# Performance work log

Measured on AMD Instinct MI355X. Metric: run time of the kernel, lower is better.

## Reference

```python
import jax, jax.numpy as jnp
import numpy as np

N = 50000        # nodes
E = 800000       # edges (avg degree 16)
C = 64           # node_dim = mid_planes = out_planes
EDGE_DIM = 16    # edge feature dim
S = 8            # share_planes


def setup_inputs() -> dict:
    key = jax.random.key(0)
    ks = jax.random.split(key, 20)

    def lin_w(k, fin, fout):
        return (jax.random.normal(k, (fin, fout), jnp.float32) / np.sqrt(fin)).astype(jnp.float32)

    return {
        "q": jax.random.normal(ks[0], (N, C), jnp.float32),
        "k": jax.random.normal(ks[1], (N, C), jnp.float32),
        "v": jax.random.normal(ks[2], (N, C), jnp.float32),
        "edges": jax.random.normal(ks[3], (E, EDGE_DIM), jnp.float32),
        "edge_index": jax.random.randint(ks[4], (E, 2), 0, N, jnp.int32),
        # linear_q / linear_k / linear_v : C -> C
        "Wq": lin_w(ks[5], C, C), "bq": jnp.zeros((C,), jnp.float32),
        "Wk": lin_w(ks[6], C, C), "bk": jnp.zeros((C,), jnp.float32),
        "Wv": lin_w(ks[7], C, C), "bv": jnp.zeros((C,), jnp.float32),
        # linear_p : EDGE_DIM -> 1
        "Wp": lin_w(ks[8], EDGE_DIM, 1), "bp": jnp.zeros((1,), jnp.float32),
        # linear_w : ReLU -> Linear(C, C//S) -> ReLU -> Linear(C//S, C//S)
        "W1": lin_w(ks[9], C, C // S), "b1": jnp.zeros((C // S,), jnp.float32),
        "W2": lin_w(ks[10], C // S, C // S), "b2": jnp.zeros((C // S,), jnp.float32),
    }


def reference(q, k, v, edges, edge_index,
              Wq, bq, Wk, bk, Wv, bv, Wp, bp, W1, b1, W2, b2):
    src = edge_index[:, 0]  # destination node of aggregation (query side)
    dst = edge_index[:, 1]  # neighbor node (key/value side)

    # node-level projections, then gather per edge
    x_q = (q @ Wq + bq)[src]            # [E, C]
    x_k = (k @ Wk + bk)[dst]            # [E, C]
    x_v = (v @ Wv + bv)[dst]            # [E, C]

    p_r = edges @ Wp + bp               # [E, 1] positional bias

    # vector attention weights (per-edge MLP)
    w = x_k - x_q + p_r                 # [E, C]
    w = jax.nn.relu(w) @ W1 + b1        # [E, C//S]
    w = jax.nn.relu(w) @ W2 + b2        # [E, C//S]
    w = jax.nn.softmax(w, axis=1)       # softmax over shared channel groups

    # weighted values, grouped by share_planes, scatter-sum back to nodes
    msg = ((x_v + p_r).reshape(E, S, C // S) * w[:, None, :]).reshape(E, C)
    return jax.ops.segment_sum(msg, src, num_segments=N)  # [N, C]
```

## Files before the change

kernel.cpp:

```cpp
#include <hip/hip_runtime.h>
#include <hip/hip_fp16.h>

#define N_NODES 50000
#define E_EDGES 800000
#define SCAN_TILE 1024
#define SCAN_NBLK ((N_NODES + SCAN_TILE - 1) / SCAN_TILE)
#define EW_EPT 8

__device__ __forceinline__ float sgpr_f(float x) {
    return __uint_as_float(__builtin_amdgcn_readfirstlane(__float_as_uint(x)));
}

#if defined(__has_builtin)
#if __has_builtin(__builtin_amdgcn_fdot2)
#define HAS_FDOT2 1
#endif
#endif

typedef _Float16 v2h_t __attribute__((ext_vector_type(2)));

__device__ __forceinline__ float fdot2f(__half2 a, __half2 b, float c) {
#ifdef HAS_FDOT2
    return __builtin_amdgcn_fdot2(*reinterpret_cast<v2h_t*>(&a),
                                  *reinterpret_cast<v2h_t*>(&b), c, false);
#else
    const float2 fa = __half22float2(a);
    const float2 fb = __half22float2(b);
    return fmaf(fa.x, fb.x, fmaf(fa.y, fb.y, c));
#endif
}

__device__ __forceinline__ __half2 relu_h2(__half2 x) {
    union { __half2 h; unsigned u; } a, r;
    a.h = x;
    asm("v_pk_max_f16 %0, %1, 0" : "=v"(r.u) : "v"(a.u));
    return r.h;
}

template <int CTRL>
__device__ __forceinline__ float dpp_mov_f32(float x) {
    return __int_as_float(__builtin_amdgcn_update_dpp(
        0, __float_as_int(x), CTRL, 0xF, 0xF, true));
}
template <int CTRL>
__device__ __forceinline__ int dpp_mov_i32(int x) {
    return __builtin_amdgcn_update_dpp(0, x, CTRL, 0xF, 0xF, true);
}
__device__ __forceinline__ float oct_sum(float x) {
    x += dpp_mov_f32<0xB1>(x);
    x += dpp_mov_f32<0x4E>(x);
    x += dpp_mov_f32<0x141>(x);
    return x;
}

__global__ __launch_bounds__(256) void proj_kernel(
    const float* __restrict__ qin, const float* __restrict__ kin, const float* __restrict__ vin,
    const float* __restrict__ Wq, const float* __restrict__ bq,
    const float* __restrict__ Wk, const float* __restrict__ bk,
    const float* __restrict__ Wv, const float* __restrict__ bv,
    __half* __restrict__ xq, __half* __restrict__ xk, __half* __restrict__ xv)
{
    __shared__ float Ws[3 * 4096];
    const int tid = threadIdx.x;
    #pragma unroll
    for (int it = 0; it < 16; ++it) {
        const int idx = it * 256 + tid;
        Ws[idx]        = Wq[idx];
        Ws[4096 + idx] = Wk[idx];
        Ws[8192 + idx] = Wv[idx];
    }
    __syncthreads();

    const int cg = tid & 15;
    const int rg = tid >> 4;
    const int c0 = cg * 4;
    const int base = blockIdx.x * 64 + rg * 4;

    const float* ins[3]  = {qin, kin, vin};
    const float* bs[3]   = {bq, bk, bv};
    __half*      outs[3] = {xq, xk, xv};

    int rowi[4];
    #pragma unroll
    for (int rr = 0; rr < 4; ++rr)
        rowi[rr] = (base + rr < N_NODES) ? (base + rr) : (N_NODES - 1);

    #pragma unroll
    for (int m = 0; m < 3; ++m) {
        const float* in = ins[m];
        const float* Wm = &Ws[m * 4096];
        float4 acc[4];
        const float4 b4 = *reinterpret_cast<const float4*>(&bs[m][c0]);
        #pragma unroll
        for (int rr = 0; rr < 4; ++rr) acc[rr] = b4;

        for (int kk = 0; kk < 64; kk += 4) {
            float4 rv[4];
            #pragma unroll
            for (int rr = 0; rr < 4; ++rr)
                rv[rr] = *reinterpret_cast<const float4*>(&in[rowi[rr] * 64 + kk]);
            #pragma unroll
            for (int dk = 0; dk < 4; ++dk) {
                const float4 w4 = *reinterpret_cast<const float4*>(&Ws[m * 4096 + (kk + dk) * 64 + c0]);
                #pragma unroll
                for (int rr = 0; rr < 4; ++rr) {
                    const float xs = reinterpret_cast<const float*>(&rv[rr])[dk];
                    acc[rr].x = fmaf(xs, w4.x, acc[rr].x);
                    acc[rr].y = fmaf(xs, w4.y, acc[rr].y);
                    acc[rr].z = fmaf(xs, w4.z, acc[rr].z);
                    acc[rr].w = fmaf(xs, w4.w, acc[rr].w);
                }
            }
        }
        #pragma unroll
        for (int rr = 0; rr < 4; ++rr) {
            if (base + rr < N_NODES) {
                union { __half2 h[2]; uint2 u; } pk;
                pk.h[0] = __floats2half2_rn(acc[rr].x, acc[rr].y);
                pk.h[1] = __floats2half2_rn(acc[rr].z, acc[rr].w);
                *reinterpret_cast<uint2*>(&outs[m][(size_t)(base + rr) * 64 + c0]) = pk.u;
            }
        }
    }
}

__global__ __launch_bounds__(256) void scan_sums(
    const int* __restrict__ cnt, int* __restrict__ bsum)
{
    const int tid  = threadIdx.x;
    const int base = blockIdx.x * SCAN_TILE + tid * 4;
    int s = 0;
    if (base + 3 < N_NODES) {
        const int4 t = *reinterpret_cast<const int4*>(&cnt[base]);
        s = t.x + t.y + t.z + t.w;
    } else {
        #pragma unroll
        for (int i = 0; i < 4; ++i)
            if (base + i < N_NODES) s += cnt[base + i];
    }
    #pragma unroll
    for (int d = 1; d < 64; d <<= 1) s += __shfl_xor(s, d);
    __shared__ int ws[4];
    if ((tid & 63) == 0) ws[tid >> 6] = s;
    __syncthreads();
    if (tid == 0) bsum[blockIdx.x] = ws[0] + ws[1] + ws[2] + ws[3];
}

__global__ __launch_bounds__(64) void scan_bsum(int* __restrict__ bsum)
{
    const int lane = threadIdx.x;
    const int v = (lane < SCAN_NBLK) ? bsum[lane] : 0;
    int incl = v;
    #pragma unroll
    for (int d = 1; d < 64; d <<= 1) {
        const int t = __shfl_up(incl, d);
        if (lane >= d) incl += t;
    }
    if (lane < SCAN_NBLK) bsum[lane] = incl - v;
}

__global__ __launch_bounds__(256) void scan_final(
    int* __restrict__ cnt, const int* __restrict__ bsum, int* __restrict__ off)
{
    const int tid  = threadIdx.x;
    const int base = blockIdx.x * SCAN_TILE + tid * 4;

    int v0 = 0, v1 = 0, v2 = 0, v3 = 0;
    if (base + 3 < N_NODES) {
        const int4 t = *reinterpret_cast<const int4*>(&cnt[base]);
        v0 = t.x; v1 = t.y; v2 = t.z; v3 = t.w;
    } else {
        if (base + 0 < N_NODES) v0 = cnt[base + 0];
        if (base + 1 < N_NODES) v1 = cnt[base + 1];
        if (base + 2 < N_NODES) v2 = cnt[base + 2];
        if (base + 3 < N_NODES) v3 = cnt[base + 3];
    }
    const int s = v0 + v1 + v2 + v3;

    int incl = s;
    #pragma unroll
    for (int d = 1; d < 64; d <<= 1) {
        const int t = __shfl_up(incl, d);
        if ((tid & 63) >= d) incl += t;
    }
    __shared__ int wsum[4];
    const int wave = tid >> 6;
    if ((tid & 63) == 63) wsum[wave] = incl;
    __syncthreads();
    int woff = 0;
    #pragma unroll
    for (int w = 0; w < 3; ++w)
        if (w < wave) woff += wsum[w];

    int run = bsum[blockIdx.x] + woff + (incl - s);
    if (base + 0 < N_NODES) { off[base + 0] = run; cnt[base + 0] = run; run += v0; }
    if (base + 1 < N_NODES) { off[base + 1] = run; cnt[base + 1] = run; run += v1; }
    if (base + 2 < N_NODES) { off[base + 2] = run; cnt[base + 2] = run; run += v2; }
    if (base + 3 < N_NODES) { off[base + 3] = run; cnt[base + 3] = run; run += v3; }

    if (blockIdx.x == 0 && tid == 0) off[N_NODES] = E_EDGES;
}

__global__ __launch_bounds__(256) void edge_weights(
    const int* __restrict__ eidx, const float* __restrict__ edges,
    const float* __restrict__ Wp, const float* __restrict__ bp,
    const float* __restrict__ W1, const float* __restrict__ b1,
    const float* __restrict__ W2, const float* __restrict__ b2,
    const __half* __restrict__ xq, const __half* __restrict__ xk,
    int* __restrict__ cnt, uint4* __restrict__ rece)
{
    const int tid  = threadIdx.x;
    const int lane = tid & 63;
    const int o    = lane >> 3;
    const int r    = lane & 7;
    const int wave = tid >> 6;

    __half2 W1h[4][8];
    #pragma unroll
    for (int i = 0; i < 4; ++i) {
        const float4 a0 = *reinterpret_cast<const float4*>(&W1[(8 * r + 2 * i) * 8]);
        const float4 a1 = *reinterpret_cast<const float4*>(&W1[(8 * r + 2 * i) * 8 + 4]);
        const float4 c0 = *reinterpret_cast<const float4*>(&W1[(8 * r + 2 * i + 1) * 8]);
        const float4 c1 = *reinterpret_cast<const float4*>(&W1[(8 * r + 2 * i + 1) * 8 + 4]);
        W1h[i][0] = __floats2half2_rn(a0.x, c0.x);
        W1h[i][1] = __floats2half2_rn(a0.y, c0.y);
        W1h[i][2] = __floats2half2_rn(a0.z, c0.z);
        W1h[i][3] = __floats2half2_rn(a0.w, c0.w);
        W1h[i][4] = __floats2half2_rn(a1.x, c1.x);
        W1h[i][5] = __floats2half2_rn(a1.y, c1.y);
        W1h[i][6] = __floats2half2_rn(a1.z, c1.z);
        W1h[i][7] = __floats2half2_rn(a1.w, c1.w);
    }
    float W2col[8];
    #pragma unroll
    for (int jj = 0; jj < 8; ++jj) W2col[jj] = W2[jj * 8 + r];
    float b1u[8];
    #pragma unroll
    for (int j = 0; j < 8; ++j) b1u[j] = sgpr_f(b1[j]);
    const float b2r = b2[r];
    const float wpA = Wp[2 * r], wpB = Wp[2 * r + 1];
    const float bp0 = sgpr_f(bp[0]);

    const int wb = (blockIdx.x * 4 + wave) * (8 * EW_EPT);

    #pragma unroll
    for (int t = 0; t < EW_EPT; ++t) {
        const int e = wb + t * 8 + o;

        const int2 sd = *reinterpret_cast<const int2*>(&eidx[2 * e]);
        const float2 e2 = *reinterpret_cast<const float2*>(&edges[(size_t)e * 16 + 2 * r]);

        uint4 q4u = *reinterpret_cast<const uint4*>(&xq[(size_t)sd.x * 64 + 8 * r]);
        uint4 k4u = *reinterpret_cast<const uint4*>(&xk[(size_t)sd.y * 64 + 8 * r]);

        float p = fmaf(e2.x, wpA, e2.y * wpB);
        p = oct_sum(p) + bp0;

        const __half2 p2 = __float2half2_rn(p);
        const __half2* qh = reinterpret_cast<const __half2*>(&q4u);
        const __half2* kh = reinterpret_cast<const __half2*>(&k4u);

        float part[8];
        #pragma unroll
        for (int jj = 0; jj < 8; ++jj) part[jj] = 0.f;
        #pragma unroll
        for (int i = 0; i < 4; ++i) {
            const __half2 d = relu_h2(__hadd2(__hsub2(kh[i], qh[i]), p2));
            #pragma unroll
            for (int jj = 0; jj < 8; ++jj)
                part[jj] = fdot2f(d, W1h[i][jj], part[jj]);
        }
        #pragma unroll
        for (int jj = 0; jj < 8; ++jj) part[jj] = oct_sum(part[jj]);

        float h2 = b2r;
        #pragma unroll
        for (int jj = 0; jj < 8; ++jj) {
            const float h1 = fmaxf(part[jj] + b1u[jj], 0.f);
            h2 = fmaf(h1, W2col[jj], h2);
        }

        const float ex = __expf(h2);
        const float sm = oct_sum(ex);
        const float w  = ex / sm;

        const unsigned wu = (unsigned)__float2uint_rn(w * 255.f);
        unsigned word = wu << (8 * (r & 3));
        word |= (unsigned)dpp_mov_i32<0xB1>((int)word);
        word |= (unsigned)dpp_mov_i32<0x4E>((int)word);
        const unsigned other = (unsigned)dpp_mov_i32<0x141>((int)word);

        if (r == 0) {
            uint4 rec;
            rec.x = (unsigned)sd.x | ((unsigned)sd.y << 16);
            rec.y = word;
            rec.z = other;
            rec.w = __float_as_uint(p);
            rece[e] = rec;
        }
        if (r == 1) atomicAdd(&cnt[sd.x], 1);
    }
}

__global__ __launch_bounds__(256) void scatter_kernel(
    const uint4* __restrict__ rece, int* __restrict__ cursor,
    uint4* __restrict__ reccsr)
{
    const int e = blockIdx.x * 256 + threadIdx.x;
    const uint4 rec = rece[e];
    const int src = (int)(rec.x & 0xFFFFu);
    const int pos = atomicAdd(&cursor[src], 1);
    reccsr[pos] = rec;
}

__global__ __launch_bounds__(256) void node_accum(
    const int* __restrict__ off, const uint4* __restrict__ reccsr,
    const __half* __restrict__ xv, float* __restrict__ out)
{
    const int tid  = threadIdx.x;
    const int lane = tid & 63;
    const int grp  = lane >> 4;
    const int sub  = (lane >> 3) & 1;
    const int r    = lane & 7;
    const int wave = tid >> 6;

    const int node = blockIdx.x * 16 + wave * 4 + grp;

    const int beg = off[node];
    const int end = off[node + 1];

    float acc[8];
    #pragma unroll
    for (int i = 0; i < 8; ++i) acc[i] = 0.f;

    int j = beg + sub;
    uint4 rec;
    if (j < end) rec = reccsr[j];

    for (; j < end; j += 2) {
        const uint4 cur = rec;
        const int   dst = (int)(cur.x >> 16);
        const float p   = __uint_as_float(cur.w);

        union { uint4 u; __half2 h[4]; } v4;
        v4.u = *reinterpret_cast<const uint4*>(&xv[(size_t)dst * 64 + 8 * r]);

        if (j + 2 < end) rec = reccsr[j + 2];

        float wf[8];
        #pragma unroll
        for (int i = 0; i < 4; ++i) {
            wf[i]     = (float)((cur.y >> (8 * i)) & 255u);
            wf[4 + i] = (float)((cur.z >> (8 * i)) & 255u);
        }

        #pragma unroll
        for (int i = 0; i < 4; ++i) {
            const float2 fv = __half22float2(v4.h[i]);
            acc[2 * i]     = fmaf(fv.x + p, wf[2 * i],     acc[2 * i]);
            acc[2 * i + 1] = fmaf(fv.y + p, wf[2 * i + 1], acc[2 * i + 1]);
        }
    }

    #pragma unroll
    for (int i = 0; i < 8; ++i)
        acc[i] += __shfl_xor(acc[i], 8);

    if (sub == 0) {
        const float c = 1.f / 255.f;
        float* orow = &out[(size_t)node * 64 + 8 * r];
        *reinterpret_cast<float4*>(orow) =
            make_float4(acc[0] * c, acc[1] * c, acc[2] * c, acc[3] * c);
        *reinterpret_cast<float4*>(orow + 4) =
            make_float4(acc[4] * c, acc[5] * c, acc[6] * c, acc[7] * c);
    }
}

extern "C" void kernel_launch(void* const* d_in, const int* in_sizes, int n_in,
                              void* d_out, int out_size, void* d_ws, size_t ws_size,
                              hipStream_t stream) {
    const float* q     = (const float*)d_in[0];
    const float* k     = (const float*)d_in[1];
    const float* v     = (const float*)d_in[2];
    const float* edges = (const float*)d_in[3];
    const int*   eidx  = (const int*)d_in[4];
    const float* Wq    = (const float*)d_in[5];
    const float* bq    = (const float*)d_in[6];
    const float* Wk    = (const float*)d_in[7];
    const float* bk    = (const float*)d_in[8];
    const float* Wv    = (const float*)d_in[9];
    const float* bv    = (const float*)d_in[10];
    const float* Wp    = (const float*)d_in[11];
    const float* bp    = (const float*)d_in[12];
    const float* W1    = (const float*)d_in[13];
    const float* b1    = (const float*)d_in[14];
    const float* W2    = (const float*)d_in[15];
    const float* b2    = (const float*)d_in[16];
    float* out = (float*)d_out;

    char* ws = (char*)d_ws;
    __half* xq = (__half*)ws;          ws += (size_t)N_NODES * 64 * sizeof(__half);
    __half* xk = (__half*)ws;          ws += (size_t)N_NODES * 64 * sizeof(__half);
    __half* xv = (__half*)ws;          ws += (size_t)N_NODES * 64 * sizeof(__half);
    int* cnt  = (int*)ws;              ws += (size_t)(N_NODES + 64) * sizeof(int);
    int* off  = (int*)ws;              ws += (size_t)(N_NODES + 64) * sizeof(int);
    int* bsum = (int*)ws;              ws += (size_t)64 * sizeof(int);
    uint4* rece   = (uint4*)ws;        ws += (size_t)E_EDGES * sizeof(uint4);
    uint4* reccsr = (uint4*)ws;        ws += (size_t)E_EDGES * sizeof(uint4);

    hipMemsetAsync(cnt, 0, (size_t)N_NODES * sizeof(int), stream);

    proj_kernel<<<dim3((N_NODES + 63) / 64), dim3(256), 0, stream>>>(
        q, k, v, Wq, bq, Wk, bk, Wv, bv, xq, xk, xv);

    edge_weights<<<dim3(E_EDGES / (32 * EW_EPT)), dim3(256), 0, stream>>>(
        eidx, edges, Wp, bp, W1, b1, W2, b2, xq, xk, cnt, rece);

    scan_sums<<<dim3(SCAN_NBLK), dim3(256), 0, stream>>>(cnt, bsum);
    scan_bsum<<<dim3(1), dim3(64), 0, stream>>>(bsum);
    scan_final<<<dim3(SCAN_NBLK), dim3(256), 0, stream>>>(cnt, bsum, off);

    scatter_kernel<<<dim3(E_EDGES / 256), dim3(256), 0, stream>>>(
        rece, cnt, reccsr);

    node_accum<<<dim3(N_NODES / 16), dim3(256), 0, stream>>>(
        off, reccsr, xv, out);
}
```

Before: 172.9 us.

## Build CSR offsets first and scatter edge records directly from edge_weights

Adds a lightweight histogram kernel over edge_index so the scan runs before edge weights are computed, letting edge_weights write each record straight to its CSR slot via the cursor atomic. This removes the intermediate per-edge record buffer and the separate scatter kernel, saving one write and one read of the record array plus a launch. Separately, the projection kernel now stores weights in LDS as packed halves and uses fdot2 on half-converted inputs, halving LDS traffic and FMA count at the cost of fp16 input rounding in the projections.

Result: no change. 171.8 us (-0.6%).

```diff
diff --git a/kernel.cpp b/kernel.cpp
--- a/kernel.cpp
+++ b/kernel.cpp
@@ -60,14 +60,24 @@
     const float* __restrict__ Wv, const float* __restrict__ bv,
     __half* __restrict__ xq, __half* __restrict__ xk, __half* __restrict__ xv)
 {
-    __shared__ float Ws[3 * 4096];
+    __shared__ unsigned Wh[3 * 2048];
     const int tid = threadIdx.x;
     #pragma unroll
-    for (int it = 0; it < 16; ++it) {
+    for (int it = 0; it < 8; ++it) {
         const int idx = it * 256 + tid;
-        Ws[idx]        = Wq[idx];
-        Ws[4096 + idx] = Wk[idx];
-        Ws[8192 + idx] = Wv[idx];
+        const int kp = idx >> 6, c = idx & 63;
+        {
+            const __half2 h = __floats2half2_rn(Wq[(2 * kp) * 64 + c], Wq[(2 * kp + 1) * 64 + c]);
+            Wh[idx] = *reinterpret_cast<const unsigned*>(&h);
+        }
+        {
+            const __half2 h = __floats2half2_rn(Wk[(2 * kp) * 64 + c], Wk[(2 * kp + 1) * 64 + c]);
+            Wh[2048 + idx] = *reinterpret_cast<const unsigned*>(&h);
+        }
+        {
+            const __half2 h = __floats2half2_rn(Wv[(2 * kp) * 64 + c], Wv[(2 * kp + 1) * 64 + c]);
+            Wh[4096 + idx] = *reinterpret_cast<const unsigned*>(&h);
+        }
     }
     __syncthreads();
 
@@ -88,27 +98,33 @@
     #pragma unroll
     for (int m = 0; m < 3; ++m) {
         const float* in = ins[m];
-        const float* Wm = &Ws[m * 4096];
         float4 acc[4];
         const float4 b4 = *reinterpret_cast<const float4*>(&bs[m][c0]);
         #pragma unroll
         for (int rr = 0; rr < 4; ++rr) acc[rr] = b4;
 
         for (int kk = 0; kk < 64; kk += 4) {
-            float4 rv[4];
+            __half2 xp[4][2];
             #pragma unroll
-            for (int rr = 0; rr < 4; ++rr)
-                rv[rr] = *reinterpret_cast<const float4*>(&in[rowi[rr] * 64 + kk]);
+            for (int rr = 0; rr < 4; ++rr) {
+                const float4 rv = *reinterpret_cast<const float4*>(&in[rowi[rr] * 64 + kk]);
+                xp[rr][0] = __floats2half2_rn(rv.x, rv.y);
+                xp[rr][1] = __floats2half2_rn(rv.z, rv.w);
+            }
             #pragma unroll
-            for (int dk = 0; dk < 4; ++dk) {
-                const float4 w4 = *reinterpret_cast<const float4*>(&Ws[m * 4096 + (kk + dk) * 64 + c0]);
+            for (int h = 0; h < 2; ++h) {
+                const int kp = (kk >> 1) + h;
+                const uint4 wq = *reinterpret_cast<const uint4*>(&Wh[m * 2048 + kp * 64 + c0]);
+                const __half2 w0 = *reinterpret_cast<const __half2*>(&wq.x);
+                const __half2 w1 = *reinterpret_cast<const __half2*>(&wq.y);
+                const __half2 w2 = *reinterpret_cast<const __half2*>(&wq.z);
+                const __half2 w3 = *reinterpret_cast<const __half2*>(&wq.w);
                 #pragma unroll
                 for (int rr = 0; rr < 4; ++rr) {
-                    const float xs = reinterpret_cast<const float*>(&rv[rr])[dk];
-                    acc[rr].x = fmaf(xs, w4.x, acc[rr].x);
-                    acc[rr].y = fmaf(xs, w4.y, acc[rr].y);
-                    acc[rr].z = fmaf(xs, w4.z, acc[rr].z);
-                    acc[rr].w = fmaf(xs, w4.w, acc[rr].w);
+                    acc[rr].x = fdot2f(xp[rr][h], w0, acc[rr].x);
+                    acc[rr].y = fdot2f(xp[rr][h], w1, acc[rr].y);
+                    acc[rr].z = fdot2f(xp[rr][h], w2, acc[rr].z);
+                    acc[rr].w = fdot2f(xp[rr][h], w3, acc[rr].w);
                 }
             }
         }
@@ -122,6 +138,13 @@
             }
         }
     }
+}
+
+__global__ __launch_bounds__(256) void hist_kernel(
+    const int* __restrict__ eidx, int* __restrict__ cnt)
+{
+    const int e = blockIdx.x * 256 + threadIdx.x;
+    atomicAdd(&cnt[eidx[2 * e]], 1);
 }
 
 __global__ __launch_bounds__(256) void scan_sums(
@@ -207,7 +230,7 @@
     const float* __restrict__ W1, const float* __restrict__ b1,
     const float* __restrict__ W2, const float* __restrict__ b2,
     const __half* __restrict__ xq, const __half* __restrict__ xk,
-    int* __restrict__ cnt, uint4* __restrict__ rece)
+    int* __restrict__ cursor, uint4* __restrict__ reccsr)
 {
     const int tid  = threadIdx.x;
     const int lane = tid & 63;
@@ -296,21 +319,10 @@
             rec.y = word;
             rec.z = other;
             rec.w = __float_as_uint(p);
-            rece[e] = rec;
-        }
-        if (r == 1) atomicAdd(&cnt[sd.x], 1);
-    }
-}
-
-__global__ __launch_bounds__(256) void scatter_kernel(
-    const uint4* __restrict__ rece, int* __restrict__ cursor,
-    uint4* __restrict__ reccsr)
-{
-    const int e = blockIdx.x * 256 + threadIdx.x;
-    const uint4 rec = rece[e];
-    const int src = (int)(rec.x & 0xFFFFu);
-    const int pos = atomicAdd(&cursor[src], 1);
-    reccsr[pos] = rec;
+            const int pos = atomicAdd(&cursor[sd.x], 1);
+            reccsr[pos] = rec;
+        }
+    }
 }
 
 __global__ __launch_bounds__(256) void node_accum(
@@ -405,23 +417,20 @@
     int* cnt  = (int*)ws;              ws += (size_t)(N_NODES + 64) * sizeof(int);
     int* off  = (int*)ws;              ws += (size_t)(N_NODES + 64) * sizeof(int);
     int* bsum = (int*)ws;              ws += (size_t)64 * sizeof(int);
-    uint4* rece   = (uint4*)ws;        ws += (size_t)E_EDGES * sizeof(uint4);
     uint4* reccsr = (uint4*)ws;        ws += (size_t)E_EDGES * sizeof(uint4);
 
     hipMemsetAsync(cnt, 0, (size_t)N_NODES * sizeof(int), stream);
 
-    proj_kernel<<<dim3((N_NODES + 63) / 64), dim3(256), 0, stream>>>(
-        q, k, v, Wq, bq, Wk, bk, Wv, bv, xq, xk, xv);
-
-    edge_weights<<<dim3(E_EDGES / (32 * EW_EPT)), dim3(256), 0, stream>>>(
-        eidx, edges, Wp, bp, W1, b1, W2, b2, xq, xk, cnt, rece);
-
+    hist_kernel<<<dim3(E_EDGES / 256), dim3(256), 0, stream>>>(eidx, cnt);
     scan_sums<<<dim3(SCAN_NBLK), dim3(256), 0, stream>>>(cnt, bsum);
     scan_bsum<<<dim3(1), dim3(64), 0, stream>>>(bsum);
     scan_final<<<dim3(SCAN_NBLK), dim3(256), 0, stream>>>(cnt, bsum, off);
 
-    scatter_kernel<<<dim3(E_EDGES / 256), dim3(256), 0, stream>>>(
-        rece, cnt, reccsr);
+    proj_kernel<<<dim3((N_NODES + 63) / 64), dim3(256), 0, stream>>>(
+        q, k, v, Wq, bq, Wk, bk, Wv, bv, xq, xk, xv);
+
+    edge_weights<<<dim3(E_EDGES / (32 * EW_EPT)), dim3(256), 0, stream>>>(
+        eidx, edges, Wp, bp, W1, b1, W2, b2, xq, xk, cnt, reccsr);
 
     node_accum<<<dim3(N_NODES / 16), dim3(256), 0, stream>>>(
         off, reccsr, xv, out);
```
